# Performance work log

Hardware: AMD Instinct MI355X
Metric: run time of the kernel (lower is better)

The kernel has to match this reference:

```python
import jax, jax.numpy as jnp
import numpy as np

V, E, H = 39, 512, 256  # vocab, emb_size, hidden_size (hard-coded in VQVAE)
B, T = 512, 128


def _p(key, shape, scale=0.05):
    return scale * jax.random.normal(key, shape, dtype=jnp.float32)


def setup_inputs() -> dict:
    key = jax.random.key(0)
    ks = jax.random.split(key, 24)
    inp = {}
    inp["input"] = jax.random.randint(ks[0], (B, T), 0, V)
    inp["src_emb_table"] = _p(ks[1], (V, E))
    inp["trg_emb_table"] = _p(ks[2], (V, E))
    # encoder bidirectional GRU (input E, hidden H), PyTorch layout (3H, in)/(3H, H)
    inp["enc_Wih_f"] = _p(ks[3], (3 * H, E)); inp["enc_Whh_f"] = _p(ks[4], (3 * H, H))
    inp["enc_bih_f"] = _p(ks[5], (3 * H,)); inp["enc_bhh_f"] = _p(ks[6], (3 * H,))
    inp["enc_Wih_b"] = _p(ks[7], (3 * H, E)); inp["enc_Whh_b"] = _p(ks[8], (3 * H, H))
    inp["enc_bih_b"] = _p(ks[9], (3 * H,)); inp["enc_bhh_b"] = _p(ks[10], (3 * H,))
    # bridge: Linear(2H -> H, bias=True)
    inp["bridge_W"] = _p(ks[11], (H, 2 * H)); inp["bridge_b"] = _p(ks[12], (H,))
    # Bahdanau attention: key (2H->H), query (H->H), energy (H->1), all bias-free
    inp["attn_Wk"] = _p(ks[13], (H, 2 * H))
    inp["attn_Wq"] = _p(ks[14], (H, H))
    inp["attn_We"] = _p(ks[15], (1, H))
    # decoder GRU (input E + 2H = 1024, hidden H)
    inp["dec_Wih"] = _p(ks[16], (3 * H, E + 2 * H)); inp["dec_Whh"] = _p(ks[17], (3 * H, H))
    inp["dec_bih"] = _p(ks[18], (3 * H,)); inp["dec_bhh"] = _p(ks[19], (3 * H,))
    # pre_output: Linear(H + 2H + E = 1280 -> H, bias=False)
    inp["pre_W"] = _p(ks[20], (H, H + 2 * H + E))
    # generator: Linear(H -> V, bias=False)
    inp["gen_W"] = _p(ks[21], (V, H))
    return inp


def gru_cell(x, h, Wih, Whh, bih, bhh):
    """PyTorch GRU cell: gates ordered [r, z, n]."""
    gi = x @ Wih.T + bih
    gh = h @ Whh.T + bhh
    ir, iz, inn = jnp.split(gi, 3, axis=-1)
    hr, hz, hn = jnp.split(gh, 3, axis=-1)
    r = jax.nn.sigmoid(ir + hr)
    z = jax.nn.sigmoid(iz + hz)
    n = jnp.tanh(inn + r * hn)
    return (1.0 - z) * n + z * h


def reference(input, src_emb_table, trg_emb_table,
              enc_Wih_f, enc_Whh_f, enc_bih_f, enc_bhh_f,
              enc_Wih_b, enc_Whh_b, enc_bih_b, enc_bhh_b,
              bridge_W, bridge_b, attn_Wk, attn_Wq, attn_We,
              dec_Wih, dec_Whh, dec_bih, dec_bhh, pre_W, gen_W):
    Bv, Tv = input.shape
    src_mask = input != 0                       # (B, T)
    trg = input[:, :-1]
    trg_y = input[:, 1:]

    # ---- Encoder: bidirectional GRU over full length (lengths == T) ----
    x = src_emb_table[input]                    # (B, T, E)
    xs = jnp.swapaxes(x, 0, 1)                  # (T, B, E)
    h0 = jnp.zeros((Bv, H), x.dtype)

    def step_f(h, xt):
        hn = gru_cell(xt, h, enc_Wih_f, enc_Whh_f, enc_bih_f, enc_bhh_f)
        return hn, hn

    def step_b(h, xt):
        hn = gru_cell(xt, h, enc_Wih_b, enc_Whh_b, enc_bih_b, enc_bhh_b)
        return hn, hn

    hf, out_f = jax.lax.scan(step_f, h0, xs)
    hb, out_b = jax.lax.scan(step_b, h0, xs[::-1])
    out_b = out_b[::-1]
    enc_out = jnp.swapaxes(jnp.concatenate([out_f, out_b], -1), 0, 1)  # (B, T, 2H)
    enc_final = jnp.concatenate([hf, hb], -1)                          # (B, 2H)

    # ---- Decoder init + precomputed attention keys ----
    hidden = jnp.tanh(enc_final @ bridge_W.T + bridge_b)               # (B, H)
    proj_key = enc_out @ attn_Wk.T                                     # (B, T, H)

    te = jnp.swapaxes(trg_emb_table[trg], 0, 1)                        # (T-1, B, E)
    neg = jnp.finfo(x.dtype).min

    def dec_step(h, prev_embed):
        q = h @ attn_Wq.T                                              # (B, H)
        e = jnp.tanh(q[:, None, :] + proj_key) @ attn_We[0]            # (B, T)
        e = jnp.where(src_mask, e, neg)
        a = jax.nn.softmax(e, axis=-1)                                 # (B, T)
        ctx = jnp.einsum('bt,btd->bd', a, enc_out)                     # (B, 2H)
        hn = gru_cell(jnp.concatenate([prev_embed, ctx], -1), h,
                      dec_Wih, dec_Whh, dec_bih, dec_bhh)              # (B, H)
        # dropout p=0.2 is identity in eval mode
        pre = jnp.concatenate([prev_embed, hn, ctx], -1) @ pre_W.T     # (B, H)
        return hn, pre

    _, pres = jax.lax.scan(dec_step, hidden, te)                       # (T-1, B, H)

    # ---- Generator + NLL loss (sum, ignore_index=0) ----
    logp = jax.nn.log_softmax(pres @ gen_W.T, axis=-1)                 # (T-1, B, V)
    ty = jnp.swapaxes(trg_y, 0, 1)                                     # (T-1, B)
    nll = -jnp.take_along_axis(logp, ty[..., None], axis=-1)[..., 0]
    loss = jnp.sum(jnp.where(ty != 0, nll, 0.0))
    return loss
```

## Files before the change

### kernel.cpp

```cpp
#include <hip/hip_runtime.h>

#define BB 512
#define TT 128
#define EE 512
#define HH 256
#define VV 39
#define H3 768
#define H2 512
#define TM1 127
#define NEGF (-3.402823466e38f)

typedef unsigned short u16;
typedef unsigned char u8;
typedef unsigned int u32;
typedef __attribute__((ext_vector_type(8))) short s16x8;
typedef __attribute__((ext_vector_type(4))) float f32x4;
typedef __attribute__((ext_vector_type(2))) unsigned int u32x2;
typedef __attribute__((ext_vector_type(4))) unsigned int u32x4;

__device__ __forceinline__ float b2f(u16 u){ u32 x=((u32)u)<<16; return __uint_as_float(x); }
__device__ __forceinline__ u16 f2b(float f){ u32 x=__float_as_uint(f); u32 r=(x+0x7fffu+((x>>16)&1u))>>16; return (u16)r; }
__device__ __forceinline__ float sigm(float x){ return 1.f/(1.f+__expf(-x)); }
__device__ __forceinline__ float tanh1(float x){ float t=__expf(2.f*x); return 1.f-2.f/(t+1.f); }
__device__ __forceinline__ float bfl(u32 u){ return __uint_as_float(u<<16); }
__device__ __forceinline__ float bfh(u32 u){ return __uint_as_float(u & 0xffff0000u); }
__device__ __forceinline__ float f8f(u32 x){
  u32 m = x & 0x7Fu;
  u32 h = ((x & 0x80u) << 8) | (m ? ((m<<4) + 0x3C00u) : 0u);
  return __uint_as_float(h << 16);
}
__device__ __forceinline__ u8 f2f8(float f){
  u32 b = __float_as_uint(f);
  u32 s = (b>>31)<<7;
  u32 mag = b & 0x7fffffffu;
  if (mag < 0x3C800000u) return (u8)s;
  u32 r = mag + 0x7FFFFu + ((mag>>20)&1u);
  if (r >= 0x43E80000u) return (u8)(s | 0x7Eu);
  u32 E = (r>>23) - 120u; u32 M = (r>>20)&7u;
  return (u8)(s | (E<<3) | M);
}

#define MFMA __builtin_amdgcn_mfma_f32_16x16x32_bf16

__device__ __forceinline__ u32 aload(const u32* p){
  return __hip_atomic_load(p, __ATOMIC_RELAXED, __HIP_MEMORY_SCOPE_AGENT);
}
__device__ __forceinline__ void astore(u32* p, u32 v){
  __hip_atomic_store(p, v, __ATOMIC_RELAXED, __HIP_MEMORY_SCOPE_AGENT);
}
#define QF(g) ((g)*16)

__global__ __launch_bounds__(256) void k_tables(
    const float* __restrict__ src_emb, const float* __restrict__ trg_emb,
    const float* __restrict__ Wih_f, const float* __restrict__ bih_f,
    const float* __restrict__ Wih_b, const float* __restrict__ bih_b,
    const float* __restrict__ dec_Wih, const float* __restrict__ dec_bih,
    const float* __restrict__ pre_W,
    float* __restrict__ tab_gi_f, float* __restrict__ tab_gi_b,
    float* __restrict__ tab_dec, float* __restrict__ tab_pre)
{
  int v = blockIdx.x;
  int y = blockIdx.y;
  int tid = threadIdx.x;
  if (y < 9){
    int seg = y/3, part = y%3;
    int n = part*256 + tid;
    const float* emb; const float* W; const float* bias; float* out; int ldw;
    if (seg==0){ emb=src_emb; W=Wih_f; bias=bih_f; out=tab_gi_f; ldw=EE; }
    else if (seg==1){ emb=src_emb; W=Wih_b; bias=bih_b; out=tab_gi_b; ldw=EE; }
    else { emb=trg_emb; W=dec_Wih; bias=dec_bih; out=tab_dec; ldw=EE+H2; }
    float acc = bias[n];
    const float* er = emb + (size_t)v*EE;
    const float* wr = W + (size_t)n*ldw;
    for (int k=0;k<EE;k++) acc += er[k]*wr[k];
    out[(size_t)v*H3 + n] = acc;
  } else {
    int n = tid;
    float acc = 0.f;
    const float* er = trg_emb + (size_t)v*EE;
    const float* wr = pre_W + (size_t)n*1280;
    for (int k=0;k<EE;k++) acc += er[k]*wr[k];
    tab_pre[(size_t)v*HH + n] = acc;
  }
}

__global__ __launch_bounds__(256) void k_cvt_all(
    const float* __restrict__ eWhh_f, const float* __restrict__ eWhh_b,
    const float* __restrict__ dWhh, const float* __restrict__ dWih,
    const float* __restrict__ Wk, const float* __restrict__ Wq,
    u16* __restrict__ o1, u16* __restrict__ o2, u16* __restrict__ o3,
    u16* __restrict__ o4, u16* __restrict__ o5, u16* __restrict__ o6)
{
  int idx = blockIdx.x*256 + threadIdx.x;
  const float* src; u16* dst; int cols, ld, off, rel;
  if      (idx <  196608){ rel=idx;          src=eWhh_f; dst=o1; cols=256; ld=256;  off=0;   }
  else if (idx <  393216){ rel=idx-196608;   src=eWhh_b; dst=o2; cols=256; ld=256;  off=0;   }
  else if (idx <  589824){ rel=idx-393216;   src=dWhh;   dst=o3; cols=256; ld=256;  off=0;   }
  else if (idx <  983040){ rel=idx-589824;   src=dWih;   dst=o4; cols=512; ld=1024; off=512; }
  else if (idx < 1114112){ rel=idx-983040;   src=Wk;     dst=o5; cols=512; ld=512;  off=0;   }
  else if (idx < 1179648){ rel=idx-1114112;  src=Wq;     dst=o6; cols=256; ld=256;  off=0;   }
  else return;
  int r = rel/cols, c2 = rel - r*cols;
  dst[rel] = f2b(src[(size_t)r*ld + off + c2]);
}

__global__ __launch_bounds__(256) void k_w2(const float* __restrict__ genW,
    const float* __restrict__ preW, u16* __restrict__ w2)
{
  int idx = blockIdx.x*256 + threadIdx.x;
  if (idx >= 64*512) return;
  int v = idx>>9, k = idx&511;
  float acc = 0.f;
  if (v < VV){
    for (int n=0;n<HH;n++) acc += genW[(size_t)v*HH+n]*preW[(size_t)n*1280+768+k];
  }
  w2[idx] = f2b(acc);
}
__global__ __launch_bounds__(256) void k_w3(const float* __restrict__ genW,
    const float* __restrict__ preW, u16* __restrict__ w3)
{
  int idx = blockIdx.x*256 + threadIdx.x;
  if (idx >= 64*256) return;
  int v = idx>>8, k = idx&255;
  float acc = 0.f;
  if (v < VV){
    for (int n=0;n<HH;n++) acc += genW[(size_t)v*HH+n]*preW[(size_t)n*1280+512+k];
  }
  w3[idx] = f2b(acc);
}
__global__ __launch_bounds__(256) void k_tlg(const float* __restrict__ tab_pre,
    const float* __restrict__ genW, float* __restrict__ tlg)
{
  int v1 = blockIdx.x, tid = threadIdx.x;
  if (tid < 64){
    float acc = 0.f;
    if (tid < VV){
      for (int n=0;n<HH;n++) acc += tab_pre[(size_t)v1*HH+n]*genW[(size_t)tid*HH+n];
    }
    tlg[(size_t)v1*64 + tid] = acc;
  }
}

__global__ __launch_bounds__(512) void k_enc_all(const int* __restrict__ input,
    const u16* __restrict__ wb_f, const u16* __restrict__ wb_b,
    const float* __restrict__ bhh_f, const float* __restrict__ bhh_b,
    const float* __restrict__ tab_f, const float* __restrict__ tab_b,
    float* __restrict__ h_f, float* __restrict__ h_b, u16* __restrict__ enc_out)
{
  __shared__ float gh[4][772];
  __shared__ u16 hs[16][264];
  int bx = blockIdx.x;
  int dirb = bx>>7, mt = bx&127;
  int m0 = mt*4;
  int tid = threadIdx.x;
  const float* tab = dirb? tab_b : tab_f;
  const float* bhh = dirb? bhh_b : bhh_f;
  const u16* Wb = dirb? wb_b : wb_f;
  int c = tid & 255, rh = tid>>8;
  float b_r=bhh[c], b_z=bhh[c+256], b_n=bhh[c+512];
  float hreg[2];
  hreg[0]=0.f; hreg[1]=0.f;
  int wv = tid>>6, lane = tid&63, l15 = lane&15, kg=(lane>>4)*8;
  int n0w = wv*96;
  float* hOut = dirb? h_b : h_f;
  { u16* z = &hs[0][0]; for (int e=tid; e<16*264; e+=512) z[e]=0; }
  __syncthreads();

  for (int s=1; s<=TT; s++){
    int tcol = dirb? (TT-s) : (s-1);
    #pragma unroll
    for (int r=0;r<2;r++){
      int row = rh*2 + r;
      int b = m0 + row;
      int tok = input[b*TT + tcol];
      const float* tg = tab + (size_t)tok*H3;
      float g0=0.f, g1=0.f, g2=0.f;
      if (s>1){ g0=gh[row][c]; g1=gh[row][c+256]; g2=gh[row][c+512]; }
      float rg = sigm(tg[c]     + g0 + b_r);
      float zg = sigm(tg[c+256] + g1 + b_z);
      float ng = tanh1(tg[c+512] + rg*(g2 + b_n));
      float hv = (1.f-zg)*ng + zg*hreg[r];
      hreg[r] = hv;
      u16 hb = f2b(hv);
      hs[row][c] = hb;
      enc_out[((size_t)b*TT + tcol)*H2 + (size_t)dirb*HH + c] = hb;
    }
    if (s==TT){
      #pragma unroll
      for (int r=0;r<2;r++)
        hOut[(size_t)(m0+rh*2+r)*HH + c] = hreg[r];
      break;
    }
    __syncthreads();
    f32x4 acc[6];
    #pragma unroll
    for (int nt=0;nt<6;nt++) acc[nt]=(f32x4){0.f,0.f,0.f,0.f};
    const u16* ar0 = &hs[l15][0];
    s16x8 bcur[6], bnext[6];
    #pragma unroll
    for (int nt=0;nt<6;nt++)
      bcur[nt] = *(const s16x8*)(Wb + (size_t)(n0w+nt*16+l15)*HH + kg);
    #pragma unroll
    for (int ko=0;ko<256;ko+=32){
      if (ko<224){
        #pragma unroll
        for (int nt=0;nt<6;nt++)
          bnext[nt] = *(const s16x8*)(Wb + (size_t)(n0w+nt*16+l15)*HH + ko+32 + kg);
      }
      s16x8 a0 = *(const s16x8*)(ar0 + ko + kg);
      #pragma unroll
      for (int nt=0;nt<6;nt++)
        acc[nt] = MFMA(a0, bcur[nt], acc[nt], 0,0,0);
      #pragma unroll
      for (int nt=0;nt<6;nt++) bcur[nt]=bnext[nt];
    }
    int q4 = (lane>>4)*4;
    if (q4 == 0){
      #pragma unroll
      for (int nt=0;nt<6;nt++){
        int col = n0w + nt*16 + l15;
        #pragma unroll
        for (int j=0;j<4;j++)
          gh[j][col] = acc[nt][j];
      }
    }
    __syncthreads();
  }
}

__global__ __launch_bounds__(256) void k_proj(const u16* __restrict__ enc,
    const u16* __restrict__ W, u16* __restrict__ out, int nTot)
{
  int m0 = blockIdx.x*64;
  int tid = threadIdx.x, wv = tid>>6, lane = tid&63;
  int l15 = lane&15, kg = (lane>>4)*8;
  int n0 = blockIdx.y*256 + wv*64;
  f32x4 acc[4][4];
  #pragma unroll
  for (int rt=0;rt<4;rt++)
    #pragma unroll
    for (int nt=0;nt<4;nt++) acc[rt][nt] = (f32x4){0.f,0.f,0.f,0.f};
  for (int ko=0; ko<512; ko+=32){
    s16x8 a[4], b[4];
    #pragma unroll
    for (int rt=0;rt<4;rt++) a[rt] = *(const s16x8*)(enc + (size_t)(m0+rt*16+l15)*H2 + ko + kg);
    #pragma unroll
    for (int nt=0;nt<4;nt++) b[nt] = *(const s16x8*)(W + (size_t)(n0+nt*16+l15)*H2 + ko + kg);
    #pragma unroll
    for (int rt=0;rt<4;rt++)
      #pragma unroll
      for (int nt=0;nt<4;nt++)
        acc[rt][nt] = MFMA(a[rt], b[nt], acc[rt][nt], 0,0,0);
  }
  #pragma unroll
  for (int rt=0;rt<4;rt++){
    int rbase = m0 + rt*16 + (lane>>4)*4;
    #pragma unroll
    for (int nt=0;nt<4;nt++){
      int col = n0 + nt*16 + l15;
      #pragma unroll
      for (int j=0;j<4;j++)
        out[(size_t)(rbase+j)*nTot + col] = f2b(acc[rt][nt][j]);
    }
  }
}

__global__ __launch_bounds__(256) void k_proj_f8(const u16* __restrict__ enc,
    const u16* __restrict__ W, u8* __restrict__ out, int nTot)
{
  int m0 = blockIdx.x*64;
  int tid = threadIdx.x, wv = tid>>6, lane = tid&63;
  int l15 = lane&15, kg = (lane>>4)*8;
  int n0 = blockIdx.y*256 + wv*64;
  f32x4 acc[4][4];
  #pragma unroll
  for (int rt=0;rt<4;rt++)
    #pragma unroll
    for (int nt=0;nt<4;nt++) acc[rt][nt] = (f32x4){0.f,0.f,0.f,0.f};
  for (int ko=0; ko<512; ko+=32){
    s16x8 a[4], b[4];
    #pragma unroll
    for (int rt=0;rt<4;rt++) a[rt] = *(const s16x8*)(enc + (size_t)(m0+rt*16+l15)*H2 + ko + kg);
    #pragma unroll
    for (int nt=0;nt<4;nt++) b[nt] = *(const s16x8*)(W + (size_t)(n0+nt*16+l15)*H2 + ko + kg);
    #pragma unroll
    for (int rt=0;rt<4;rt++)
      #pragma unroll
      for (int nt=0;nt<4;nt++)
        acc[rt][nt] = MFMA(a[rt], b[nt], acc[rt][nt], 0,0,0);
  }
  #pragma unroll
  for (int rt=0;rt<4;rt++){
    int rbase = m0 + rt*16 + (lane>>4)*4;
    #pragma unroll
    for (int nt=0;nt<4;nt++){
      int col = n0 + nt*16 + l15;
      #pragma unroll
      for (int j=0;j<4;j++)
        out[(size_t)(rbase+j)*nTot + col] = f2f8(acc[rt][nt][j]);
    }
  }
}

__global__ __launch_bounds__(256) void k_proj64(const u16* __restrict__ enc,
    const u16* __restrict__ W2, u16* __restrict__ out)
{
  int m0 = blockIdx.x*64;
  int tid = threadIdx.x, wv = tid>>6, lane = tid&63;
  int l15 = lane&15, kg = (lane>>4)*8;
  int n0 = wv*16;
  f32x4 acc[4];
  #pragma unroll
  for (int rt=0;rt<4;rt++) acc[rt] = (f32x4){0.f,0.f,0.f,0.f};
  for (int ko=0; ko<512; ko+=32){
    s16x8 b = *(const s16x8*)(W2 + (size_t)(n0+l15)*H2 + ko + kg);
    #pragma unroll
    for (int rt=0;rt<4;rt++){
      s16x8 a = *(const s16x8*)(enc + (size_t)(m0+rt*16+l15)*H2 + ko + kg);
      acc[rt] = MFMA(a, b, acc[rt], 0,0,0);
    }
  }
  #pragma unroll
  for (int rt=0;rt<4;rt++){
    int rbase = m0 + rt*16 + (lane>>4)*4;
    int col = n0 + l15;
    #pragma unroll
    for (int j=0;j<4;j++)
      out[(size_t)(rbase+j)*64 + col] = f2b(acc[rt][j]);
  }
}

__global__ __launch_bounds__(256) void k_bridge(const float* __restrict__ h_f,
    const float* __restrict__ h_b, const float* __restrict__ bw,
    const float* __restrict__ bb, float* __restrict__ hst)
{
  __shared__ float As[32][68];
  __shared__ float Ws[32][68];
  int n0=blockIdx.x*64, m0=blockIdx.y*64, tid=threadIdx.x;
  int ar=tid>>2, ak=(tid&3)*8;
  int rt=tid>>4, ct=tid&15;
  float acc[4][4];
  #pragma unroll
  for (int j=0;j<4;j++){
    #pragma unroll
    for (int l=0;l<4;l++) acc[j][l]=0.f;
  }
  for (int ko=0;ko<512;ko+=32){
    int k0=ko+ak;
    const float* asrc = (k0<256)? (h_f + (size_t)(m0+ar)*HH + k0)
                                : (h_b + (size_t)(m0+ar)*HH + (k0-256));
    float4 a0=*(const float4*)asrc, a1=*(const float4*)(asrc+4);
    const float* wsrc = bw + (size_t)(n0+ar)*H2 + k0;
    float4 w0=*(const float4*)wsrc, w1=*(const float4*)(wsrc+4);
    __syncthreads();
    As[ak+0][ar]=a0.x; As[ak+1][ar]=a0.y; As[ak+2][ar]=a0.z; As[ak+3][ar]=a0.w;
    As[ak+4][ar]=a1.x; As[ak+5][ar]=a1.y; As[ak+6][ar]=a1.z; As[ak+7][ar]=a1.w;
    Ws[ak+0][ar]=w0.x; Ws[ak+1][ar]=w0.y; Ws[ak+2][ar]=w0.z; Ws[ak+3][ar]=w0.w;
    Ws[ak+4][ar]=w1.x; Ws[ak+5][ar]=w1.y; Ws[ak+6][ar]=w1.z; Ws[ak+7][ar]=w1.w;
    __syncthreads();
    #pragma unroll
    for (int kk=0;kk<32;kk++){
      float4 a=*(const float4*)&As[kk][rt*4];
      float4 w=*(const float4*)&Ws[kk][ct*4];
      float a4[4]={a.x,a.y,a.z,a.w};
      float w4[4]={w.x,w.y,w.z,w.w};
      #pragma unroll
      for (int j=0;j<4;j++){
        #pragma unroll
        for (int l=0;l<4;l++) acc[j][l]+=a4[j]*w4[l];
      }
    }
  }
  #pragma unroll
  for (int j=0;j<4;j++){
    int row=m0+rt*4+j;
    #pragma unroll
    for (int l=0;l<4;l++){
      int col=n0+ct*4+l;
      hst[(size_t)row*HH+col]=tanh1(acc[j][l]+bb[col]);
    }
  }
}

__global__ __launch_bounds__(256) void k_boot(
    const float* __restrict__ hst, const u16* __restrict__ whh,
    const u16* __restrict__ wq, float* __restrict__ ghg,
    float* __restrict__ qg, float* __restrict__ nll)
{
  __shared__ u16 hsb[16][264];
  int bx=blockIdx.x, tid=threadIdx.x;
  int wv=tid>>6, lane=tid&63, l15=lane&15, kg=(lane>>4)*8;
  int b0=bx*16;
  {
    int c=tid;
    for (int r=0;r<16;r++) hsb[r][c] = f2b(hst[(size_t)(b0+r)*HH + c]);
  }
  if (tid<16) nll[b0+tid] = 0.f;
  __syncthreads();
  int rr = (lane>>4)*4;
  for (int nt=0;nt<12;nt++){
    int n0 = wv*192 + nt*16;
    f32x4 acc = (f32x4){0.f,0.f,0.f,0.f};
    for (int ko=0;ko<256;ko+=32){
      s16x8 a = *(const s16x8*)&hsb[l15][ko+kg];
      s16x8 bf = *(const s16x8*)(whh + (size_t)(n0+l15)*HH + ko + kg);
      acc = MFMA(a, bf, acc, 0,0,0);
    }
    #pragma unroll
    for (int jr=0;jr<4;jr++)
      ghg[(size_t)(b0+rr+jr)*H3 + n0 + l15] = acc[jr];
  }
  #pragma unroll
  for (int nt=0;nt<4;nt++){
    int n0 = wv*64 + nt*16;
    f32x4 acc = (f32x4){0.f,0.f,0.f,0.f};
    for (int ko=0;ko<256;ko+=32){
      s16x8 a = *(const s16x8*)&hsb[l15][ko+kg];
      s16x8 bf = *(const s16x8*)(wq + (size_t)(n0+l15)*HH + ko + kg);
      acc = MFMA(a, bf, acc, 0,0,0);
    }
    #pragma unroll
    for (int jr=0;jr<4;jr++)
      qg[(size_t)(b0+rr+jr)*HH + n0 + l15] = acc[jr];
  }
}

__global__ __launch_bounds__(512,4) void k_step(int L,
    const int* __restrict__ input,
    const float* __restrict__ tab_dec, const float* __restrict__ tab_lgt,
    const float* __restrict__ bhh, const float* __restrict__ We,
    const u16* __restrict__ whh, const u16* __restrict__ wq,
    const u16* __restrict__ w3,
    const u16* __restrict__ pk, const u8* __restrict__ eih8,
    const u16* __restrict__ e2,
    float* __restrict__ hst, u32* __restrict__ qgu, float* __restrict__ ghg,
    u16* __restrict__ gicW, const u16* __restrict__ gicR,
    u16* __restrict__ lgcW, const u16* __restrict__ lgcR,
    float* __restrict__ nll, u32* __restrict__ fl)
{
  __shared__ __align__(16) char smem[40960];
  u16 (*gicL)[776] = (u16(*)[776])smem;
  u16 (*lgcL)[64]  = (u16(*)[64])(smem+24832);
  u16 (*hsb)[264]  = (u16(*)[264])(smem+26880);
  float (*lgt)[64] = (float(*)[64])(smem+35328);
  int* stokG       = (int*)(smem+39424);
  float* aL  = (float*)smem;
  int* stok  = (int*)(smem+512);
  float* qS  = (float*)(smem+1024);
  float (*pG)[768] = (float(*)[768])(smem+4096);
  float (*pE)[64]  = (float(*)[64])(smem+28672);

  int bx=blockIdx.x, tid=threadIdx.x;
  int wv=tid>>6, lane=tid&63, l15=lane&15, kg=(lane>>4)*8;

  if (bx < 32 && L > 0){
    int s = L-1;
    int b0 = bx*16;
    int rr = (lane>>4)*4;
    float b_r, b_z, b_n;
    { int c=tid&255; b_r=bhh[c]; b_z=bhh[c+256]; b_n=bhh[c+512]; }
    for (int idx=tid; idx<6144; idx+=512){
      int r = idx/384, k = idx - r*384;
      *(u32*)&gicL[r][2*k] = *(const u32*)(gicR + (size_t)(b0+r)*H3 + 2*k);
    }
    { int r=tid>>5, k=tid&31;
      *(u32*)&lgcL[r][2*k] = *(const u32*)(lgcR + (size_t)(b0+r)*64 + 2*k); }
    if (tid<16) stokG[tid] = input[(b0+tid)*TT + s];
    __syncthreads();
    {
      int c = tid&255, rh = tid>>8;
      for (int r=rh*8; r<rh*8+8; r++){
        int bb = b0+r;
        const float* tg = tab_dec + (size_t)stokG[r]*H3;
        const float* gr = ghg + (size_t)bb*H3;
        float rg = sigm(tg[c]     + b2f(gicL[r][c])     + gr[c]     + b_r);
        float zg = sigm(tg[c+256] + b2f(gicL[r][c+256]) + gr[c+256] + b_z);
        float ng = tanh1(tg[c+512] + b2f(gicL[r][c+512]) + rg*(gr[c+512] + b_n));
        float hv = (1.f-zg)*ng + zg*hst[(size_t)bb*HH + c];
        hst[(size_t)bb*HH + c] = hv;
        hsb[r][c] = f2b(hv);
      }
    }
    __syncthreads();
    {
      f32x4 accq[2];
      accq[0]=(f32x4){0.f,0.f,0.f,0.f}; accq[1]=(f32x4){0.f,0.f,0.f,0.f};
      #pragma unroll
      for (int ko=0;ko<256;ko+=32){
        s16x8 bq0 = *(const s16x8*)(wq + (size_t)(wv*32+l15)*HH + ko + kg);
        s16x8 bq1 = *(const s16x8*)(wq + (size_t)(wv*32+16+l15)*HH + ko + kg);
        s16x8 a = *(const s16x8*)&hsb[l15][ko+kg];
        accq[0] = MFMA(a,bq0,accq[0],0,0,0);
        accq[1] = MFMA(a,bq1,accq[1],0,0,0);
      }
      #pragma unroll
      for (int nt=0;nt<2;nt++)
        #pragma unroll
        for (int jr=0;jr<4;jr++)
          astore(qgu + (size_t)(b0+rr+jr)*HH + wv*32+nt*16+l15,
                 __float_as_uint(accq[nt][jr]));
    }
    __syncthreads();
    if (tid==0) astore(&fl[QF(bx)], (u32)L);
    {
      f32x4 acc6[6];
      #pragma unroll
      for (int nt=0;nt<6;nt++) acc6[nt]=(f32x4){0.f,0.f,0.f,0.f};
      #pragma unroll
      for (int ko=0;ko<256;ko+=32){
        s16x8 b6[6];
        #pragma unroll
        for (int nt=0;nt<6;nt++)
          b6[nt] = *(const s16x8*)(whh + (size_t)(wv*96+nt*16+l15)*HH + ko + kg);
        s16x8 a = *(const s16x8*)&hsb[l15][ko+kg];
        #pragma unroll
        for (int nt=0;nt<6;nt++) acc6[nt]=MFMA(a,b6[nt],acc6[nt],0,0,0);
      }
      #pragma unroll
      for (int nt=0;nt<6;nt++)
        #pragma unroll
        for (int jr=0;jr<4;jr++)
          ghg[(size_t)(b0+rr+jr)*H3 + wv*96+nt*16+l15] = acc6[nt][jr];
    }
    if (wv<4){
      int n0 = wv*16;
      f32x4 acc = (f32x4){0.f,0.f,0.f,0.f};
      for (int ko=0;ko<256;ko+=32){
        s16x8 a = *(const s16x8*)&hsb[l15][ko+kg];
        s16x8 bf = *(const s16x8*)(w3 + (size_t)(n0+l15)*HH + ko + kg);
        acc = MFMA(a,bf,acc,0,0,0);
      }
      #pragma unroll
      for (int jr=0;jr<4;jr++){
        int r = rr+jr, col = n0+l15;
        lgt[r][col] = acc[jr] + tab_lgt[(size_t)stokG[r]*64 + col]
                    + b2f(lgcL[r][col]);
      }
    }
    __syncthreads();
    {
      int r = wv*4 + (lane>>4);
      if (r < 16){
        float v0 = lgt[r][l15];
        float v1 = lgt[r][l15+16];
        float v2 = (l15<7)? lgt[r][l15+32] : NEGF;
        float m = fmaxf(fmaxf(v0,v1),v2);
        #pragma unroll
        for (int off=8; off; off>>=1) m = fmaxf(m, __shfl_xor(m,off));
        float pe = __expf(v0-m) + __expf(v1-m) + ((l15<7)? __expf(v2-m) : 0.f);
        #pragma unroll
        for (int off=8; off; off>>=1) pe += __shfl_xor(pe,off);
        if (l15==0){
          int ty = input[(b0+r)*TT + s+1];
          if (ty != 0) nll[b0+r] += m + __logf(pe) - lgt[r][ty];
        }
      }
    }
    __syncthreads();
  }

  if (L < TM1){
    int r2 = bx;
    int g2 = r2>>4;
    int l32 = lane&31;
    if (tid < TT) stok[tid] = input[r2*TT + tid];
    const u16* pkb = pk + (size_t)r2*TT*HH + l32*8;
    s16x8 kv[8];
    #pragma unroll
    for (int it=0; it<8; it++){
      int t = wv*16 + it*2 + (lane>>5);
      kv[it] = *(const s16x8*)(pkb + (size_t)t*HH);
    }
    float4 w0 = *(const float4*)(We + l32*8);
    float4 w1 = *(const float4*)(We + l32*8 + 4);
    __syncthreads();
    if (L > 0){
      if (tid==0){
        while (aload(&fl[QF(g2)]) < (u32)L) __builtin_amdgcn_s_sleep(1);
      }
      __syncthreads();
    }
    if (tid < 256) qS[tid] = __uint_as_float(aload(qgu + (size_t)r2*HH + tid));
    __syncthreads();
    float4 q0 = *(const float4*)&qS[l32*8];
    float4 q1 = *(const float4*)&qS[l32*8 + 4];
    #pragma unroll
    for (int it=0; it<8; it++){
      int t = wv*16 + it*2 + (lane>>5);
      s16x8 k8 = kv[it];
      float sE = tanh1(q0.x + b2f((u16)k8[0]))*w0.x
               + tanh1(q0.y + b2f((u16)k8[1]))*w0.y
               + tanh1(q0.z + b2f((u16)k8[2]))*w0.z
               + tanh1(q0.w + b2f((u16)k8[3]))*w0.w
               + tanh1(q1.x + b2f((u16)k8[4]))*w1.x
               + tanh1(q1.y + b2f((u16)k8[5]))*w1.y
               + tanh1(q1.z + b2f((u16)k8[6]))*w1.z
               + tanh1(q1.w + b2f((u16)k8[7]))*w1.w;
      #pragma unroll
      for (int off=16; off; off>>=1) sE += __shfl_xor(sE, off);
      if (l32==0) aL[t] = stok[t] ? sE : NEGF;
    }
    __syncthreads();
    if (wv==0){
      float v0 = aL[lane], v1 = aL[64+lane];
      float m = fmaxf(v0,v1);
      #pragma unroll
      for (int off=32; off; off>>=1) m = fmaxf(m, __shfl_xor(m,off));
      float p0 = __expf(v0-m), p1 = __expf(v1-m);
      float sS = p0+p1;
      #pragma unroll
      for (int off=32; off; off>>=1) sS += __shfl_xor(sS,off);
      float inv = 1.f/sS;
      aL[lane] = p0*inv; aL[64+lane] = p1*inv;
    }
    __syncthreads();
    {
      float gA[8], gB[4], eA=0.f;
      #pragma unroll
      for (int e=0;e<8;e++) gA[e]=0.f;
      #pragma unroll
      for (int e=0;e<4;e++) gB[e]=0.f;
      const u8* ei = eih8 + (size_t)r2*TT*H3;
      const u16* ee = e2 + (size_t)r2*TT*64;
      int t0 = wv*16;
      #pragma unroll 4
      for (int tt=0; tt<16; tt++){
        int t = t0+tt;
        float a = aL[t];
        u32x2 v0 = *(const u32x2*)(ei + (size_t)t*H3 + lane*8);
        u32 v1 = *(const u32*)(ei + (size_t)t*H3 + 512 + lane*4);
        float ev = b2f(ee[(size_t)t*64 + lane]);
        gA[0]+=a*f8f(v0.x); gA[1]+=a*f8f(v0.x>>8);
        gA[2]+=a*f8f(v0.x>>16); gA[3]+=a*f8f(v0.x>>24);
        gA[4]+=a*f8f(v0.y); gA[5]+=a*f8f(v0.y>>8);
        gA[6]+=a*f8f(v0.y>>16); gA[7]+=a*f8f(v0.y>>24);
        gB[0]+=a*f8f(v1); gB[1]+=a*f8f(v1>>8);
        gB[2]+=a*f8f(v1>>16); gB[3]+=a*f8f(v1>>24);
        eA += a*ev;
      }
      #pragma unroll
      for (int e=0;e<8;e++) pG[wv][lane*8+e] = gA[e];
      #pragma unroll
      for (int e=0;e<4;e++) pG[wv][512+lane*4+e] = gB[e];
      pE[wv][lane] = eA;
    }
    __syncthreads();
    if (tid < 384){
      float lo=0.f, hi=0.f;
      #pragma unroll
      for (int w=0;w<8;w++){ lo += pG[w][2*tid]; hi += pG[w][2*tid+1]; }
      u32 v = (u32)f2b(lo) | ((u32)f2b(hi)<<16);
      *(u32*)&gicW[(size_t)r2*H3 + 2*tid] = v;
    } else if (tid < 416){
      int d = tid-384;
      float lo=0.f, hi=0.f;
      #pragma unroll
      for (int w=0;w<8;w++){ lo += pE[w][2*d]; hi += pE[w][2*d+1]; }
      u32 v = (u32)f2b(lo) | ((u32)f2b(hi)<<16);
      *(u32*)&lgcW[(size_t)r2*64 + 2*d] = v;
    }
  }
}

__global__ __launch_bounds__(256) void k_loss(const float* __restrict__ nll,
                                              float* __restrict__ out)
{
  __shared__ float sm[256];
  int tid=threadIdx.x;
  float s = nll[tid] + nll[tid+256];
  sm[tid]=s; __syncthreads();
  for (int off=128; off; off>>=1){
    if (tid<off) sm[tid]+=sm[tid+off];
    __syncthreads();
  }
  if (tid==0) out[0]=sm[0];
}

extern "C" void kernel_launch(void* const* d_in, const int* in_sizes, int n_in,
                              void* d_out, int out_size, void* d_ws, size_t ws_size,
                              hipStream_t stream)
{
  const int*   input    = (const int*)  d_in[0];
  const float* src_emb  = (const float*)d_in[1];
  const float* trg_emb  = (const float*)d_in[2];
  const float* eWih_f   = (const float*)d_in[3];
  const float* eWhh_f   = (const float*)d_in[4];
  const float* ebih_f   = (const float*)d_in[5];
  const float* ebhh_f   = (const float*)d_in[6];
  const float* eWih_b   = (const float*)d_in[7];
  const float* eWhh_b   = (const float*)d_in[8];
  const float* ebih_b   = (const float*)d_in[9];
  const float* ebhh_b   = (const float*)d_in[10];
  const float* bridge_W = (const float*)d_in[11];
  const float* bridge_b = (const float*)d_in[12];
  const float* attn_Wk  = (const float*)d_in[13];
  const float* attn_Wq  = (const float*)d_in[14];
  const float* attn_We  = (const float*)d_in[15];
  const float* dec_Wih  = (const float*)d_in[16];
  const float* dec_Whh  = (const float*)d_in[17];
  const float* dec_bih  = (const float*)d_in[18];
  const float* dec_bhh  = (const float*)d_in[19];
  const float* pre_W    = (const float*)d_in[20];
  const float* gen_W    = (const float*)d_in[21];

  float* F = (float*)d_ws;
  size_t o=0;
  u32* fl         = (u32*)(F+o); o+=2048;
  float* tab_gi_f = F+o; o+=(size_t)VV*H3;
  float* tab_gi_b = F+o; o+=(size_t)VV*H3;
  float* tab_dec  = F+o; o+=(size_t)VV*H3;
  float* tab_pre  = F+o; o+=(size_t)VV*HH;
  float* tab_lgt  = F+o; o+=(size_t)VV*64;
  float* h_f      = F+o; o+=(size_t)BB*HH;
  float* h_b      = F+o; o+=(size_t)BB*HH;
  float* hst      = F+o; o+=(size_t)BB*HH;
  float* qg       = F+o; o+=(size_t)BB*HH;
  float* ghg      = F+o; o+=(size_t)BB*H3;
  float* nll      = F+o; o+=(size_t)BB;
  u16* U = (u16*)(F+o);
  size_t uo=0;
  u16* enc_out = U+uo; uo+=(size_t)BB*TT*H2;
  u16* pk      = U+uo; uo+=(size_t)BB*TT*HH;
  u16* e2      = U+uo; uo+=(size_t)BB*TT*64;
  u16* gic0    = U+uo; uo+=(size_t)BB*H3;
  u16* gic1    = U+uo; uo+=(size_t)BB*H3;
  u16* lgc0    = U+uo; uo+=(size_t)BB*64;
  u16* lgc1    = U+uo; uo+=(size_t)BB*64;
  u16* wb_ehh_f= U+uo; uo+=(size_t)H3*HH;
  u16* wb_ehh_b= U+uo; uo+=(size_t)H3*HH;
  u16* wb_dhh  = U+uo; uo+=(size_t)H3*HH;
  u16* wb_dih  = U+uo; uo+=(size_t)H3*H2;
  u16* wb_wk   = U+uo; uo+=(size_t)HH*H2;
  u16* wb_wq   = U+uo; uo+=(size_t)HH*HH;
  u16* wb_w2   = U+uo; uo+=(size_t)64*H2;
  u16* wb_w3   = U+uo; uo+=(size_t)64*HH;
  u8* eih8 = (u8*)(U+uo);

  dim3 blk(256,1,1);
  k_tables<<<dim3(VV,10),blk,0,stream>>>(src_emb,trg_emb,eWih_f,ebih_f,eWih_b,ebih_b,
                                         dec_Wih,dec_bih,pre_W,
                                         tab_gi_f,tab_gi_b,tab_dec,tab_pre);
  k_tlg<<<dim3(VV),blk,0,stream>>>(tab_pre,gen_W,tab_lgt);
  k_cvt_all<<<dim3(4608),blk,0,stream>>>(eWhh_f,eWhh_b,dec_Whh,dec_Wih,attn_Wk,attn_Wq,
                                         wb_ehh_f,wb_ehh_b,wb_dhh,wb_dih,wb_wk,wb_wq);
  k_w2<<<dim3(128),blk,0,stream>>>(gen_W,pre_W,wb_w2);
  k_w3<<<dim3(64),blk,0,stream>>>(gen_W,pre_W,wb_w3);
  k_enc_all<<<dim3(256),dim3(512),0,stream>>>(input,wb_ehh_f,wb_ehh_b,ebhh_f,ebhh_b,
                                              tab_gi_f,tab_gi_b,h_f,h_b,enc_out);
  k_proj<<<dim3(1024,1),blk,0,stream>>>(enc_out,wb_wk,pk,HH);
  k_proj_f8<<<dim3(1024,3),blk,0,stream>>>(enc_out,wb_dih,eih8,H3);
  k_proj64<<<dim3(1024),blk,0,stream>>>(enc_out,wb_w2,e2);
  k_bridge<<<dim3(4,8),blk,0,stream>>>(h_f,h_b,bridge_W,bridge_b,hst);
  k_boot<<<dim3(32),blk,0,stream>>>(hst,wb_dhh,wb_wq,ghg,qg,nll);
  hipMemsetAsync(fl, 0, 8192, stream);

  for (int L=0; L<=TM1; L++){
    u16* gw = (L&1)? gic1 : gic0;
    u16* gr = (L&1)? gic0 : gic1;
    u16* lw = (L&1)? lgc1 : lgc0;
    u16* lr = (L&1)? lgc0 : lgc1;
    k_step<<<dim3(512),dim3(512),0,stream>>>(L,input,tab_dec,tab_lgt,dec_bhh,attn_We,
                                             wb_dhh,wb_wq,wb_w3,
                                             pk,eih8,e2,hst,(u32*)qg,ghg,
                                             gw,gr,lw,lr,nll,fl);
  }
  k_loss<<<dim3(1),blk,0,stream>>>(nll,(float*)d_out);
}
```

Baseline: 7.982 ms.

## Replace per-step decoder launches with one persistent kernel owning two batch rows

Drops the 128 per-timestep launches of k_step, the k_boot kernel and the flag-based cross-block spin synchronisation. One kernel of 256 blocks now runs the whole 127-step decoder, each block owning two batch rows. Hidden state, gate pre-activations, query, context projections and attention keys stay in shared memory or registers across steps, removing global round trips and launch overhead. The cost is MFMA tiles that use only 2 of 16 rows. Every block also re-reads the Whh, Wq and W3 weights from cache at every step.

```diff
diff --git a/kernel.cpp b/kernel.cpp
--- a/kernel.cpp
+++ b/kernel.cpp
@@ -41,14 +41,6 @@
 }
 
 #define MFMA __builtin_amdgcn_mfma_f32_16x16x32_bf16
-
-__device__ __forceinline__ u32 aload(const u32* p){
-  return __hip_atomic_load(p, __ATOMIC_RELAXED, __HIP_MEMORY_SCOPE_AGENT);
-}
-__device__ __forceinline__ void astore(u32* p, u32 v){
-  __hip_atomic_store(p, v, __ATOMIC_RELAXED, __HIP_MEMORY_SCOPE_AGENT);
-}
-#define QF(g) ((g)*16)
 
 __global__ __launch_bounds__(256) void k_tables(
     const float* __restrict__ src_emb, const float* __restrict__ trg_emb,
@@ -382,227 +374,119 @@
   }
 }
 
-__global__ __launch_bounds__(256) void k_boot(
-    const float* __restrict__ hst, const u16* __restrict__ whh,
-    const u16* __restrict__ wq, float* __restrict__ ghg,
-    float* __restrict__ qg, float* __restrict__ nll)
-{
-  __shared__ u16 hsb[16][264];
-  int bx=blockIdx.x, tid=threadIdx.x;
-  int wv=tid>>6, lane=tid&63, l15=lane&15, kg=(lane>>4)*8;
-  int b0=bx*16;
-  {
-    int c=tid;
-    for (int r=0;r<16;r++) hsb[r][c] = f2b(hst[(size_t)(b0+r)*HH + c]);
-  }
-  if (tid<16) nll[b0+tid] = 0.f;
-  __syncthreads();
-  int rr = (lane>>4)*4;
-  for (int nt=0;nt<12;nt++){
-    int n0 = wv*192 + nt*16;
-    f32x4 acc = (f32x4){0.f,0.f,0.f,0.f};
-    for (int ko=0;ko<256;ko+=32){
-      s16x8 a = *(const s16x8*)&hsb[l15][ko+kg];
-      s16x8 bf = *(const s16x8*)(whh + (size_t)(n0+l15)*HH + ko + kg);
-      acc = MFMA(a, bf, acc, 0,0,0);
-    }
-    #pragma unroll
-    for (int jr=0;jr<4;jr++)
-      ghg[(size_t)(b0+rr+jr)*H3 + n0 + l15] = acc[jr];
-  }
-  #pragma unroll
-  for (int nt=0;nt<4;nt++){
-    int n0 = wv*64 + nt*16;
-    f32x4 acc = (f32x4){0.f,0.f,0.f,0.f};
-    for (int ko=0;ko<256;ko+=32){
-      s16x8 a = *(const s16x8*)&hsb[l15][ko+kg];
-      s16x8 bf = *(const s16x8*)(wq + (size_t)(n0+l15)*HH + ko + kg);
-      acc = MFMA(a, bf, acc, 0,0,0);
-    }
-    #pragma unroll
-    for (int jr=0;jr<4;jr++)
-      qg[(size_t)(b0+rr+jr)*HH + n0 + l15] = acc[jr];
-  }
-}
-
-__global__ __launch_bounds__(512,4) void k_step(int L,
+__global__ __launch_bounds__(512,1) void k_dec_rows(
     const int* __restrict__ input,
     const float* __restrict__ tab_dec, const float* __restrict__ tab_lgt,
     const float* __restrict__ bhh, const float* __restrict__ We,
     const u16* __restrict__ whh, const u16* __restrict__ wq,
     const u16* __restrict__ w3,
     const u16* __restrict__ pk, const u8* __restrict__ eih8,
-    const u16* __restrict__ e2,
-    float* __restrict__ hst, u32* __restrict__ qgu, float* __restrict__ ghg,
-    u16* __restrict__ gicW, const u16* __restrict__ gicR,
-    u16* __restrict__ lgcW, const u16* __restrict__ lgcR,
-    float* __restrict__ nll, u32* __restrict__ fl)
-{
-  __shared__ __align__(16) char smem[40960];
-  u16 (*gicL)[776] = (u16(*)[776])smem;
-  u16 (*lgcL)[64]  = (u16(*)[64])(smem+24832);
-  u16 (*hsb)[264]  = (u16(*)[264])(smem+26880);
-  float (*lgt)[64] = (float(*)[64])(smem+35328);
-  int* stokG       = (int*)(smem+39424);
-  float* aL  = (float*)smem;
-  int* stok  = (int*)(smem+512);
-  float* qS  = (float*)(smem+1024);
-  float (*pG)[768] = (float(*)[768])(smem+4096);
-  float (*pE)[64]  = (float(*)[64])(smem+28672);
-
-  int bx=blockIdx.x, tid=threadIdx.x;
-  int wv=tid>>6, lane=tid&63, l15=lane&15, kg=(lane>>4)*8;
-
-  if (bx < 32 && L > 0){
-    int s = L-1;
-    int b0 = bx*16;
-    int rr = (lane>>4)*4;
-    float b_r, b_z, b_n;
-    { int c=tid&255; b_r=bhh[c]; b_z=bhh[c+256]; b_n=bhh[c+512]; }
-    for (int idx=tid; idx<6144; idx+=512){
-      int r = idx/384, k = idx - r*384;
-      *(u32*)&gicL[r][2*k] = *(const u32*)(gicR + (size_t)(b0+r)*H3 + 2*k);
-    }
-    { int r=tid>>5, k=tid&31;
-      *(u32*)&lgcL[r][2*k] = *(const u32*)(lgcR + (size_t)(b0+r)*64 + 2*k); }
-    if (tid<16) stokG[tid] = input[(b0+tid)*TT + s];
-    __syncthreads();
+    const u16* __restrict__ e2, const float* __restrict__ hst,
+    float* __restrict__ nll)
+{
+  __shared__ float hL[2][HH];
+  __shared__ u16 hsb[16][264];
+  __shared__ float ghL[2][H3];
+  __shared__ float qS[2][HH];
+  __shared__ float gicS[2][H3];
+  __shared__ float lgcS[2][64];
+  __shared__ float aL[2][TT];
+  __shared__ float pG[8][768];
+  __shared__ float pE[8][64];
+  __shared__ float lgt[2][64];
+  __shared__ int stokD[2][TT];
+
+  int bx = blockIdx.x, tid = threadIdx.x;
+  int wv = tid>>6, lane = tid&63, l15 = lane&15, kg = (lane>>4)*8;
+  int rowA = bx*2;
+  int rsel = wv>>2, wl = wv&3;
+  int rT = tid>>8, cT = tid&255;
+
+  { u16* z = &hsb[0][0]; for (int e=tid; e<16*264; e+=512) z[e]=0; }
+  if (tid < 256) stokD[tid>>7][tid&127] = input[(rowA+(tid>>7))*TT + (tid&127)];
+  {
+    float hv = hst[(size_t)(rowA+rT)*HH + cT];
+    hL[rT][cT] = hv;
+  }
+  float b_r = bhh[cT], b_z = bhh[cT+256], b_n = bhh[cT+512];
+  float4 weL = *(const float4*)(We + lane*4);
+  u32x2 kv[32];
+  {
+    const u16* pkb = pk + ((size_t)(rowA+rsel)*TT + wl*32)*HH + lane*4;
+    #pragma unroll
+    for (int tt=0; tt<32; tt++)
+      kv[tt] = *(const u32x2*)(pkb + (size_t)tt*HH);
+  }
+  float nlacc = 0.f;
+  __syncthreads();
+  hsb[rT][cT] = f2b(hL[rT][cT]);
+  __syncthreads();
+
+  #define GHQ_PHASE(DO_GH)                                                    \
+  {                                                                           \
+    if (DO_GH){                                                               \
+      f32x4 acc6[6];                                                          \
+      _Pragma("unroll")                                                       \
+      for (int nt=0;nt<6;nt++) acc6[nt]=(f32x4){0.f,0.f,0.f,0.f};             \
+      _Pragma("unroll")                                                       \
+      for (int ko=0;ko<256;ko+=32){                                           \
+        s16x8 b6[6];                                                          \
+        _Pragma("unroll")                                                     \
+        for (int nt=0;nt<6;nt++)                                              \
+          b6[nt] = *(const s16x8*)(whh + (size_t)(wv*96+nt*16+l15)*HH + ko + kg); \
+        s16x8 a = *(const s16x8*)&hsb[l15][ko+kg];                            \
+        _Pragma("unroll")                                                     \
+        for (int nt=0;nt<6;nt++) acc6[nt]=MFMA(a,b6[nt],acc6[nt],0,0,0);      \
+      }                                                                       \
+      if ((lane>>4)==0){                                                      \
+        _Pragma("unroll")                                                     \
+        for (int nt=0;nt<6;nt++){                                             \
+          int col = wv*96+nt*16+l15;                                          \
+          ghL[0][col] = acc6[nt][0];                                          \
+          ghL[1][col] = acc6[nt][1];                                          \
+        }                                                                     \
+      }                                                                       \
+    }                                                                         \
+    {                                                                         \
+      f32x4 accq[2];                                                          \
+      accq[0]=(f32x4){0.f,0.f,0.f,0.f}; accq[1]=(f32x4){0.f,0.f,0.f,0.f};     \
+      _Pragma("unroll")                                                       \
+      for (int ko=0;ko<256;ko+=32){                                           \
+        s16x8 bq0 = *(const s16x8*)(wq + (size_t)(wv*32+l15)*HH + ko + kg);   \
+        s16x8 bq1 = *(const s16x8*)(wq + (size_t)(wv*32+16+l15)*HH + ko + kg);\
+        s16x8 a = *(const s16x8*)&hsb[l15][ko+kg];                            \
+        accq[0] = MFMA(a,bq0,accq[0],0,0,0);                                  \
+        accq[1] = MFMA(a,bq1,accq[1],0,0,0);                                  \
+      }                                                                       \
+      if ((lane>>4)==0){                                                      \
+        _Pragma("unroll")                                                     \
+        for (int nt=0;nt<2;nt++){                                             \
+          int col = wv*32+nt*16+l15;                                          \
+          qS[0][col] = accq[nt][0];                                           \
+          qS[1][col] = accq[nt][1];                                           \
+        }                                                                     \
+      }                                                                       \
+    }                                                                         \
+  }
+  GHQ_PHASE(1)
+  __syncthreads();
+
+  for (int j=0; j<TM1; j++){
     {
-      int c = tid&255, rh = tid>>8;
-      for (int r=rh*8; r<rh*8+8; r++){
-        int bb = b0+r;
-        const float* tg = tab_dec + (size_t)stokG[r]*H3;
-        const float* gr = ghg + (size_t)bb*H3;
-        float rg = sigm(tg[c]     + b2f(gicL[r][c])     + gr[c]     + b_r);
-        float zg = sigm(tg[c+256] + b2f(gicL[r][c+256]) + gr[c+256] + b_z);
-        float ng = tanh1(tg[c+512] + b2f(gicL[r][c+512]) + rg*(gr[c+512] + b_n));
-        float hv = (1.f-zg)*ng + zg*hst[(size_t)bb*HH + c];
-        hst[(size_t)bb*HH + c] = hv;
-        hsb[r][c] = f2b(hv);
-      }
-    }
-    __syncthreads();
-    {
-      f32x4 accq[2];
-      accq[0]=(f32x4){0.f,0.f,0.f,0.f}; accq[1]=(f32x4){0.f,0.f,0.f,0.f};
-      #pragma unroll
-      for (int ko=0;ko<256;ko+=32){
-        s16x8 bq0 = *(const s16x8*)(wq + (size_t)(wv*32+l15)*HH + ko + kg);
-        s16x8 bq1 = *(const s16x8*)(wq + (size_t)(wv*32+16+l15)*HH + ko + kg);
-        s16x8 a = *(const s16x8*)&hsb[l15][ko+kg];
-        accq[0] = MFMA(a,bq0,accq[0],0,0,0);
-        accq[1] = MFMA(a,bq1,accq[1],0,0,0);
-      }
-      #pragma unroll
-      for (int nt=0;nt<2;nt++)
+      float4 qq = *(const float4*)&qS[rsel][lane*4];
+      #pragma unroll 4
+      for (int tt=0; tt<32; tt++){
+        u32x2 pp = kv[tt];
+        float sE = tanh1(qq.x+bfl(pp.x))*weL.x + tanh1(qq.y+bfh(pp.x))*weL.y
+                 + tanh1(qq.z+bfl(pp.y))*weL.z + tanh1(qq.w+bfh(pp.y))*weL.w;
         #pragma unroll
-        for (int jr=0;jr<4;jr++)
-          astore(qgu + (size_t)(b0+rr+jr)*HH + wv*32+nt*16+l15,
-                 __float_as_uint(accq[nt][jr]));
-    }
-    __syncthreads();
-    if (tid==0) astore(&fl[QF(bx)], (u32)L);
-    {
-      f32x4 acc6[6];
-      #pragma unroll
-      for (int nt=0;nt<6;nt++) acc6[nt]=(f32x4){0.f,0.f,0.f,0.f};
-      #pragma unroll
-      for (int ko=0;ko<256;ko+=32){
-        s16x8 b6[6];
-        #pragma unroll
-        for (int nt=0;nt<6;nt++)
-          b6[nt] = *(const s16x8*)(whh + (size_t)(wv*96+nt*16+l15)*HH + ko + kg);
-        s16x8 a = *(const s16x8*)&hsb[l15][ko+kg];
-        #pragma unroll
-        for (int nt=0;nt<6;nt++) acc6[nt]=MFMA(a,b6[nt],acc6[nt],0,0,0);
-      }
-      #pragma unroll
-      for (int nt=0;nt<6;nt++)
-        #pragma unroll
-        for (int jr=0;jr<4;jr++)
-          ghg[(size_t)(b0+rr+jr)*H3 + wv*96+nt*16+l15] = acc6[nt][jr];
-    }
-    if (wv<4){
-      int n0 = wv*16;
-      f32x4 acc = (f32x4){0.f,0.f,0.f,0.f};
-      for (int ko=0;ko<256;ko+=32){
-        s16x8 a = *(const s16x8*)&hsb[l15][ko+kg];
-        s16x8 bf = *(const s16x8*)(w3 + (size_t)(n0+l15)*HH + ko + kg);
-        acc = MFMA(a,bf,acc,0,0,0);
-      }
-      #pragma unroll
-      for (int jr=0;jr<4;jr++){
-        int r = rr+jr, col = n0+l15;
-        lgt[r][col] = acc[jr] + tab_lgt[(size_t)stokG[r]*64 + col]
-                    + b2f(lgcL[r][col]);
-      }
-    }
-    __syncthreads();
-    {
-      int r = wv*4 + (lane>>4);
-      if (r < 16){
-        float v0 = lgt[r][l15];
-        float v1 = lgt[r][l15+16];
-        float v2 = (l15<7)? lgt[r][l15+32] : NEGF;
-        float m = fmaxf(fmaxf(v0,v1),v2);
-        #pragma unroll
-        for (int off=8; off; off>>=1) m = fmaxf(m, __shfl_xor(m,off));
-        float pe = __expf(v0-m) + __expf(v1-m) + ((l15<7)? __expf(v2-m) : 0.f);
-        #pragma unroll
-        for (int off=8; off; off>>=1) pe += __shfl_xor(pe,off);
-        if (l15==0){
-          int ty = input[(b0+r)*TT + s+1];
-          if (ty != 0) nll[b0+r] += m + __logf(pe) - lgt[r][ty];
-        }
-      }
-    }
-    __syncthreads();
-  }
-
-  if (L < TM1){
-    int r2 = bx;
-    int g2 = r2>>4;
-    int l32 = lane&31;
-    if (tid < TT) stok[tid] = input[r2*TT + tid];
-    const u16* pkb = pk + (size_t)r2*TT*HH + l32*8;
-    s16x8 kv[8];
-    #pragma unroll
-    for (int it=0; it<8; it++){
-      int t = wv*16 + it*2 + (lane>>5);
-      kv[it] = *(const s16x8*)(pkb + (size_t)t*HH);
-    }
-    float4 w0 = *(const float4*)(We + l32*8);
-    float4 w1 = *(const float4*)(We + l32*8 + 4);
-    __syncthreads();
-    if (L > 0){
-      if (tid==0){
-        while (aload(&fl[QF(g2)]) < (u32)L) __builtin_amdgcn_s_sleep(1);
-      }
-      __syncthreads();
-    }
-    if (tid < 256) qS[tid] = __uint_as_float(aload(qgu + (size_t)r2*HH + tid));
-    __syncthreads();
-    float4 q0 = *(const float4*)&qS[l32*8];
-    float4 q1 = *(const float4*)&qS[l32*8 + 4];
-    #pragma unroll
-    for (int it=0; it<8; it++){
-      int t = wv*16 + it*2 + (lane>>5);
-      s16x8 k8 = kv[it];
-      float sE = tanh1(q0.x + b2f((u16)k8[0]))*w0.x
-               + tanh1(q0.y + b2f((u16)k8[1]))*w0.y
-               + tanh1(q0.z + b2f((u16)k8[2]))*w0.z
-               + tanh1(q0.w + b2f((u16)k8[3]))*w0.w
-               + tanh1(q1.x + b2f((u16)k8[4]))*w1.x
-               + tanh1(q1.y + b2f((u16)k8[5]))*w1.y
-               + tanh1(q1.z + b2f((u16)k8[6]))*w1.z
-               + tanh1(q1.w + b2f((u16)k8[7]))*w1.w;
-      #pragma unroll
-      for (int off=16; off; off>>=1) sE += __shfl_xor(sE, off);
-      if (l32==0) aL[t] = stok[t] ? sE : NEGF;
-    }
-    __syncthreads();
-    if (wv==0){
-      float v0 = aL[lane], v1 = aL[64+lane];
+        for (int off=32; off; off>>=1) sE += __shfl_xor(sE, off);
+        if (lane==0) aL[rsel][wl*32+tt] = stokD[rsel][wl*32+tt] ? sE : NEGF;
+      }
+    }
+    __syncthreads();
+    if (wl==0){
+      float v0 = aL[rsel][lane], v1 = aL[rsel][64+lane];
       float m = fmaxf(v0,v1);
       #pragma unroll
       for (int off=32; off; off>>=1) m = fmaxf(m, __shfl_xor(m,off));
@@ -611,25 +495,25 @@
       #pragma unroll
       for (int off=32; off; off>>=1) sS += __shfl_xor(sS,off);
       float inv = 1.f/sS;
-      aL[lane] = p0*inv; aL[64+lane] = p1*inv;
+      aL[rsel][lane] = p0*inv; aL[rsel][64+lane] = p1*inv;
     }
     __syncthreads();
     {
-      float gA[8], gB[4], eA=0.f;
+      float gA[8], gB[4], eA = 0.f;
       #pragma unroll
       for (int e=0;e<8;e++) gA[e]=0.f;
       #pragma unroll
       for (int e=0;e<4;e++) gB[e]=0.f;
-      const u8* ei = eih8 + (size_t)r2*TT*H3;
-      const u16* ee = e2 + (size_t)r2*TT*64;
-      int t0 = wv*16;
+      const u8* ei = eih8 + (size_t)(rowA+rsel)*TT*H3;
+      const u16* ee = e2 + (size_t)(rowA+rsel)*TT*64;
+      int t0 = wl*32;
       #pragma unroll 4
-      for (int tt=0; tt<16; tt++){
+      for (int tt=0; tt<32; tt++){
         int t = t0+tt;
-        float a = aL[t];
+        float a = aL[rsel][t];
         u32x2 v0 = *(const u32x2*)(ei + (size_t)t*H3 + lane*8);
         u32 v1 = *(const u32*)(ei + (size_t)t*H3 + 512 + lane*4);
-        float ev = b2f(ee[(size_t)t*64 + lane]);
+        float ev = b2f(ee[(size_t)t*64 + (lane&63)]);
         gA[0]+=a*f8f(v0.x); gA[1]+=a*f8f(v0.x>>8);
         gA[2]+=a*f8f(v0.x>>16); gA[3]+=a*f8f(v0.x>>24);
         gA[4]+=a*f8f(v0.y); gA[5]+=a*f8f(v0.y>>8);
@@ -645,21 +529,66 @@
       pE[wv][lane] = eA;
     }
     __syncthreads();
-    if (tid < 384){
-      float lo=0.f, hi=0.f;
-      #pragma unroll
-      for (int w=0;w<8;w++){ lo += pG[w][2*tid]; hi += pG[w][2*tid+1]; }
-      u32 v = (u32)f2b(lo) | ((u32)f2b(hi)<<16);
-      *(u32*)&gicW[(size_t)r2*H3 + 2*tid] = v;
-    } else if (tid < 416){
-      int d = tid-384;
-      float lo=0.f, hi=0.f;
-      #pragma unroll
-      for (int w=0;w<8;w++){ lo += pE[w][2*d]; hi += pE[w][2*d+1]; }
-      u32 v = (u32)f2b(lo) | ((u32)f2b(hi)<<16);
-      *(u32*)&lgcW[(size_t)r2*64 + 2*d] = v;
-    }
-  }
+    for (int idx=tid; idx<1536; idx+=512){
+      int r = idx/768, k = idx - r*768;
+      int base = r*4;
+      gicS[r][k] = pG[base][k]+pG[base+1][k]+pG[base+2][k]+pG[base+3][k];
+    }
+    if (tid < 128){
+      int r = tid>>6, k = tid&63;
+      int base = r*4;
+      lgcS[r][k] = pE[base][k]+pE[base+1][k]+pE[base+2][k]+pE[base+3][k];
+    }
+    __syncthreads();
+    {
+      int tok = stokD[rT][j];
+      const float* tg = tab_dec + (size_t)tok*H3;
+      float rg = sigm(tg[cT]     + gicS[rT][cT]     + ghL[rT][cT]     + b_r);
+      float zg = sigm(tg[cT+256] + gicS[rT][cT+256] + ghL[rT][cT+256] + b_z);
+      float ng = tanh1(tg[cT+512] + gicS[rT][cT+512] + rg*(ghL[rT][cT+512] + b_n));
+      float hv = (1.f-zg)*ng + zg*hL[rT][cT];
+      hL[rT][cT] = hv;
+      hsb[rT][cT] = f2b(hv);
+    }
+    __syncthreads();
+    if (wv < 4){
+      int n0 = wv*16;
+      f32x4 acc = (f32x4){0.f,0.f,0.f,0.f};
+      #pragma unroll
+      for (int ko=0;ko<256;ko+=32){
+        s16x8 a = *(const s16x8*)&hsb[l15][ko+kg];
+        s16x8 bf = *(const s16x8*)(w3 + (size_t)(n0+l15)*HH + ko + kg);
+        acc = MFMA(a,bf,acc,0,0,0);
+      }
+      if ((lane>>4)==0){
+        #pragma unroll
+        for (int jr=0;jr<2;jr++){
+          int col = n0+l15;
+          lgt[jr][col] = acc[jr] + tab_lgt[(size_t)stokD[jr][j]*64 + col]
+                       + lgcS[jr][col];
+        }
+      }
+    }
+    GHQ_PHASE(1)
+    __syncthreads();
+    if (wv < 2){
+      float v0 = lgt[wv][l15];
+      float v1 = lgt[wv][l15+16];
+      float v2 = (l15<7)? lgt[wv][l15+32] : NEGF;
+      float m = fmaxf(fmaxf(v0,v1),v2);
+      #pragma unroll
+      for (int off=8; off; off>>=1) m = fmaxf(m, __shfl_xor(m,off));
+      float pe = __expf(v0-m) + __expf(v1-m) + ((l15<7)? __expf(v2-m) : 0.f);
+      #pragma unroll
+      for (int off=8; off; off>>=1) pe += __shfl_xor(pe,off);
+      if (lane==0){
+        int ty = stokD[wv][j+1];
+        if (ty != 0) nlacc += m + __logf(pe) - lgt[wv][ty];
+      }
+    }
+    __syncthreads();
+  }
+  if (wv < 2 && lane == 0) nll[rowA + wv] = nlacc;
 }
 
 __global__ __launch_bounds__(256) void k_loss(const float* __restrict__ nll,
@@ -705,7 +634,6 @@
 
   float* F = (float*)d_ws;
   size_t o=0;
-  u32* fl         = (u32*)(F+o); o+=2048;
   float* tab_gi_f = F+o; o+=(size_t)VV*H3;
   float* tab_gi_b = F+o; o+=(size_t)VV*H3;
   float* tab_dec  = F+o; o+=(size_t)VV*H3;
@@ -714,18 +642,12 @@
   float* h_f      = F+o; o+=(size_t)BB*HH;
   float* h_b      = F+o; o+=(size_t)BB*HH;
   float* hst      = F+o; o+=(size_t)BB*HH;
-  float* qg       = F+o; o+=(size_t)BB*HH;
-  float* ghg      = F+o; o+=(size_t)BB*H3;
   float* nll      = F+o; o+=(size_t)BB;
   u16* U = (u16*)(F+o);
   size_t uo=0;
   u16* enc_out = U+uo; uo+=(size_t)BB*TT*H2;
   u16* pk      = U+uo; uo+=(size_t)BB*TT*HH;
   u16* e2      = U+uo; uo+=(size_t)BB*TT*64;
-  u16* gic0    = U+uo; uo+=(size_t)BB*H3;
-  u16* gic1    = U+uo; uo+=(size_t)BB*H3;
-  u16* lgc0    = U+uo; uo+=(size_t)BB*64;
-  u16* lgc1    = U+uo; uo+=(size_t)BB*64;
   u16* wb_ehh_f= U+uo; uo+=(size_t)H3*HH;
   u16* wb_ehh_b= U+uo; uo+=(size_t)H3*HH;
   u16* wb_dhh  = U+uo; uo+=(size_t)H3*HH;
@@ -751,18 +673,8 @@
   k_proj_f8<<<dim3(1024,3),blk,0,stream>>>(enc_out,wb_dih,eih8,H3);
   k_proj64<<<dim3(1024),blk,0,stream>>>(enc_out,wb_w2,e2);
   k_bridge<<<dim3(4,8),blk,0,stream>>>(h_f,h_b,bridge_W,bridge_b,hst);
-  k_boot<<<dim3(32),blk,0,stream>>>(hst,wb_dhh,wb_wq,ghg,qg,nll);
-  hipMemsetAsync(fl, 0, 8192, stream);
-
-  for (int L=0; L<=TM1; L++){
-    u16* gw = (L&1)? gic1 : gic0;
-    u16* gr = (L&1)? gic0 : gic1;
-    u16* lw = (L&1)? lgc1 : lgc0;
-    u16* lr = (L&1)? lgc0 : lgc1;
-    k_step<<<dim3(512),dim3(512),0,stream>>>(L,input,tab_dec,tab_lgt,dec_bhh,attn_We,
-                                             wb_dhh,wb_wq,wb_w3,
-                                             pk,eih8,e2,hst,(u32*)qg,ghg,
-                                             gw,gr,lw,lr,nll,fl);
-  }
+  k_dec_rows<<<dim3(256),dim3(512),0,stream>>>(input,tab_dec,tab_lgt,dec_bhh,attn_We,
+                                               wb_dhh,wb_wq,wb_w3,
+                                               pk,eih8,e2,hst,nll);
   k_loss<<<dim3(1),blk,0,stream>>>(nll,(float*)d_out);
 }
```

Result: slower. 8.774 ms (+9.9%).
